# Kernel optimization log

Measured on AMD Instinct MI355X. Metric: run time of the kernel, lower is better.

The kernel has to match this reference:

```python
import jax, jax.numpy as jnp
import numpy as np

TAU = 0.2        # temperature
LAM = 0.5        # lambda_weight
P = 128          # proj_dim


def l2n(x):
    # tf.math.l2_normalize semantics: x / sqrt(max(sum(x^2), eps))
    return x / jnp.sqrt(jnp.maximum(jnp.sum(x * x, axis=-1, keepdims=True), 1e-12))


def global_head(feat, W1, b1, W2, b2):
    # GlobalAveragePooling2D -> Dense(2048, relu) -> Dense(128); dropout is identity in eval
    g = jnp.mean(feat, axis=(1, 2))                       # [B, C]
    return jax.nn.relu(g @ W1 + b1) @ W2 + b2             # [B, 128]


def dense_head(feat, W1, b1, W2, b2):
    # 1x1 Conv2D(2048, relu) -> 1x1 Conv2D(128) == per-pixel matmuls
    h = jax.nn.relu(jnp.einsum('bhwc,cd->bhwd', feat, W1) + b1)
    return jnp.einsum('bhwd,de->bhwe', h, W2) + b2        # [B, H, W, 128]


def dense_correspondence(q, k):
    b, h, w, c = q.shape
    f1 = q.reshape(b, h * w, c)
    f2 = k.reshape(b, h * w, c)
    sim = jnp.einsum('bnc,bmc->bnm', f1, f2)              # [B, hw, hw]
    idx = jnp.argmax(sim, axis=-1)                        # [B, hw]
    return jnp.take_along_axis(f2, idx[:, :, None], axis=1)  # batched gather


def info_nce(q, k):
    logits = (q @ k.T) / TAU                              # [N, N]
    lse = jax.nn.logsumexp(logits, axis=-1)
    pos = jnp.diagonal(logits)                            # labels = arange(N)
    return jnp.mean(lse - pos)


def queue_info_nce(q, k, queue):
    l_pos = jnp.sum(q * k, axis=-1, keepdims=True)        # [B, 1]
    l_neg = q @ queue.T                                   # [B, Q]
    logits = jnp.concatenate([l_pos, l_neg], axis=1) / TAU
    # labels are all zero -> positive logit is column 0
    return jnp.mean(jax.nn.logsumexp(logits, axis=-1) - logits[:, 0])


def setup_inputs() -> dict:
    key = jax.random.key(0)
    ks = jax.random.split(key, 16)
    B, H, W, C, D = 8, 28, 28, 1024, 2048
    Q = 65536
    s1 = 0.02
    inp = {
        'feat_q': jax.random.normal(ks[0], (B, H, W, C), jnp.float32),
        'feat_k': jax.random.normal(ks[1], (B, H, W, C), jnp.float32),
        'Wg1': jax.random.normal(ks[2], (C, D), jnp.float32) * s1,
        'bg1': jnp.zeros((D,), jnp.float32),
        'Wg2': jax.random.normal(ks[3], (D, P), jnp.float32) * s1,
        'bg2': jnp.zeros((P,), jnp.float32),
        'Wd1': jax.random.normal(ks[4], (C, D), jnp.float32) * s1,
        'bd1': jnp.zeros((D,), jnp.float32),
        'Wd2': jax.random.normal(ks[5], (D, P), jnp.float32) * s1,
        'bd2': jnp.zeros((P,), jnp.float32),
        'mWg1': jax.random.normal(ks[6], (C, D), jnp.float32) * s1,
        'mbg1': jnp.zeros((D,), jnp.float32),
        'mWg2': jax.random.normal(ks[7], (D, P), jnp.float32) * s1,
        'mbg2': jnp.zeros((P,), jnp.float32),
        'mWd1': jax.random.normal(ks[8], (C, D), jnp.float32) * s1,
        'mbd1': jnp.zeros((D,), jnp.float32),
        'mWd2': jax.random.normal(ks[9], (D, P), jnp.float32) * s1,
        'mbd2': jnp.zeros((P,), jnp.float32),
        'queue': l2n(jax.random.normal(ks[10], (Q, P), jnp.float32)),
    }
    return inp


def reference(feat_q, feat_k, Wg1, bg1, Wg2, bg2, Wd1, bd1, Wd2, bd2,
              mWg1, mbg1, mWg2, mbg2, mWd1, mbd1, mWd2, mbd2, queue):
    # student branch
    q_g = l2n(global_head(feat_q, Wg1, bg1, Wg2, bg2))
    q_d = l2n(dense_head(feat_q, Wd1, bd1, Wd2, bd2))
    # momentum (teacher) branch, stop-gradient as in train_step
    k_g = jax.lax.stop_gradient(l2n(global_head(feat_k, mWg1, mbg1, mWg2, mbg2)))
    k_d = jax.lax.stop_gradient(l2n(dense_head(feat_k, mWd1, mbd1, mWd2, mbd2)))
    # post-warmup path (warmup_epochs=0)
    l_g = queue_info_nce(q_g, k_g, queue)
    matched_k = dense_correspondence(q_d, k_d)
    l_d = info_nce(q_d.reshape(-1, P), matched_k.reshape(-1, P))
    total = (1.0 - LAM) * l_g + LAM * l_d
    return total
```

## Files before the change

### kernel.cpp

```cpp
#include <hip/hip_runtime.h>
#include <cstdint>

#define TAU_INV 5.0f
#define L2E 1.4426950408889634f

using ushort = unsigned short;
typedef __attribute__((ext_vector_type(8))) short s16x8;
typedef __attribute__((ext_vector_type(4))) float f32x4;

static __device__ __forceinline__ ushort f2bf(float x) {
  unsigned u = __float_as_uint(x);
  return (ushort)((u + 0x7fffu + ((u >> 16) & 1u)) >> 16);
}

static __device__ __forceinline__ float fexp2(float x) {
#if __has_builtin(__builtin_amdgcn_exp2f)
  return __builtin_amdgcn_exp2f(x);
#else
  return exp2f(x);
#endif
}

static __device__ __forceinline__ void gload_lds16(const void* g, void* l) {
  __builtin_amdgcn_global_load_lds(
      reinterpret_cast<const __attribute__((address_space(1))) void*>(
          reinterpret_cast<uintptr_t>(g)),
      reinterpret_cast<__attribute__((address_space(3))) void*>(
          (unsigned)reinterpret_cast<uintptr_t>(l)),
      16, 0, 0);
}

static __device__ __forceinline__ void xcd_swizzle(int gx, int gy, int& bx, int& by) {
  int nwg = gx * gy;
  int flat = by * gx + bx;
  int q = nwg >> 3, r = nwg & 7;
  int xcd = flat & 7, sl = flat >> 3;
  int tile = (xcd < r ? xcd * (q + 1) : r * (q + 1) + (xcd - r) * q) + sl;
  by = tile / gx;
  bx = tile - by * gx;
}

__global__ void k_cvt_pool(const float* __restrict__ fq, const float* __restrict__ fk,
                           ushort* __restrict__ obf, float* __restrict__ gpart) {
  int br = blockIdx.y >> 3, b = blockIdx.y & 7, pc = blockIdx.x, t = threadIdx.x;
  const float* feat = br ? fk : fq;
  const float* fp = feat + ((size_t)b * 784 + (size_t)pc * 7) * 1024;
  ushort* op = obf + (size_t)br * 6422528 + ((size_t)b * 784 + (size_t)pc * 7) * 1024;
  float4 acc = {0.f, 0.f, 0.f, 0.f};
#pragma unroll
  for (int p = 0; p < 7; ++p) {
    float4 v = ((const float4*)(fp + (size_t)p * 1024))[t];
    acc.x += v.x; acc.y += v.y; acc.z += v.z; acc.w += v.w;
    ushort4 r;
    r.x = f2bf(v.x); r.y = f2bf(v.y); r.z = f2bf(v.z); r.w = f2bf(v.w);
    ((ushort4*)(op + (size_t)p * 1024))[t] = r;
  }
  ((float4*)(gpart + ((size_t)blockIdx.y * 112 + pc) * 1024))[t] = acc;
}

__global__ void k_gpool_fin(const float* __restrict__ gpart, float* __restrict__ g) {
  int idx = blockIdx.x * 256 + threadIdx.x;
  int bb = idx >> 10, c = idx & 1023;
  float s = 0.f;
#pragma unroll 4
  for (int pc = 0; pc < 112; ++pc) s += gpart[((size_t)bb * 112 + pc) * 1024 + c];
  g[idx] = s * (1.0f / 784.0f);
}

__global__ void k_dense1_part(const float* __restrict__ g, const float* __restrict__ W0,
                              const float* __restrict__ W1, float* __restrict__ part1) {
  int br = blockIdx.z;
  const float* gb = g + (size_t)br * 8192;
  const float* W = br ? W1 : W0;
  float* p1 = part1 + (size_t)br * 262144;
  int d = blockIdx.x * 256 + threadIdx.x;
  int k0 = blockIdx.y * 64;
  __shared__ float gs[512];
  for (int i = threadIdx.x; i < 512; i += 256) gs[i] = gb[(i >> 6) * 1024 + k0 + (i & 63)];
  __syncthreads();
  float acc[8] = {};
  for (int kk = 0; kk < 64; ++kk) {
    float w = W[(size_t)(k0 + kk) * 2048 + d];
#pragma unroll
    for (int b = 0; b < 8; ++b) acc[b] += gs[b * 64 + kk] * w;
  }
#pragma unroll
  for (int b = 0; b < 8; ++b) p1[((size_t)blockIdx.y * 8 + b) * 2048 + d] = acc[b];
}

__global__ void k_d12(const float* __restrict__ part1, const float* __restrict__ b10,
                      const float* __restrict__ b11, const float* __restrict__ W20,
                      const float* __restrict__ W21, float* __restrict__ part2) {
  int br = blockIdx.y, k0 = blockIdx.x * 64;
  const float* p1 = part1 + (size_t)br * 262144;
  const float* b1 = br ? b11 : b10;
  const float* W2 = br ? W21 : W20;
  float* p2 = part2 + (size_t)br * 32768;
  __shared__ float hs[512];
  for (int i = threadIdx.x; i < 512; i += 128) {
    int b = i >> 6, kk = i & 63;
    float s = b1[k0 + kk];
#pragma unroll
    for (int ks = 0; ks < 16; ++ks) s += p1[((size_t)ks * 8 + b) * 2048 + k0 + kk];
    hs[i] = fmaxf(s, 0.f);
  }
  __syncthreads();
  int d = threadIdx.x;
  float acc[8] = {};
  for (int kk = 0; kk < 64; ++kk) {
    float w = W2[(size_t)(k0 + kk) * 128 + d];
#pragma unroll
    for (int b = 0; b < 8; ++b) acc[b] += hs[b * 64 + kk] * w;
  }
#pragma unroll
  for (int b = 0; b < 8; ++b) p2[((size_t)blockIdx.x * 8 + b) * 128 + d] = acc[b];
}

__global__ void k_head_fin(const float* __restrict__ p2q, const float* __restrict__ p2k,
                           const float* __restrict__ bq, const float* __restrict__ bk,
                           float* __restrict__ qg, float* __restrict__ kg,
                           float* __restrict__ lpos) {
  int b = blockIdx.x, lane = threadIdx.x;
  float q0 = bq[lane], q1 = bq[lane + 64];
  float k0 = bk[lane], k1 = bk[lane + 64];
#pragma unroll
  for (int s = 0; s < 32; ++s) {
    size_t base = ((size_t)s * 8 + b) * 128;
    q0 += p2q[base + lane]; q1 += p2q[base + lane + 64];
    k0 += p2k[base + lane]; k1 += p2k[base + lane + 64];
  }
  float sq = q0 * q0 + q1 * q1, sk = k0 * k0 + k1 * k1;
#pragma unroll
  for (int d = 1; d < 64; d <<= 1) { sq += __shfl_xor(sq, d); sk += __shfl_xor(sk, d); }
  float rq = 1.0f / sqrtf(fmaxf(sq, 1e-12f));
  float rk = 1.0f / sqrtf(fmaxf(sk, 1e-12f));
  q0 *= rq; q1 *= rq; k0 *= rk; k1 *= rk;
  qg[b * 128 + lane] = q0; qg[b * 128 + 64 + lane] = q1;
  kg[b * 128 + lane] = k0; kg[b * 128 + 64 + lane] = k1;
  float lp = q0 * k0 + q1 * k1;
#pragma unroll
  for (int d = 1; d < 64; d <<= 1) lp += __shfl_xor(lp, d);
  if (lane == 0) lpos[b] = lp;
}

__global__ void k_transpose_all(const float* __restrict__ Wd1, const float* __restrict__ mWd1,
                                const float* __restrict__ Wd2, const float* __restrict__ mWd2,
                                ushort* __restrict__ Wt1, ushort* __restrict__ Wt2) {
  int fl = blockIdx.x, z = blockIdx.z;
  const float* W;
  ushort* o;
  int bx, by, K, N;
  if (fl < 2048) {
    W = z ? mWd1 : Wd1;
    o = Wt1 + (size_t)z * 2097152;
    bx = fl & 63; by = fl >> 6; K = 1024; N = 2048;
  } else {
    fl -= 2048;
    W = z ? mWd2 : Wd2;
    o = Wt2 + (size_t)z * 262144;
    bx = fl & 3; by = fl >> 2; K = 2048; N = 128;
  }
  __shared__ float tile[32][33];
  int n0 = bx * 32, k0 = by * 32;
  int tx = threadIdx.x & 31, ty = threadIdx.x >> 5;
#pragma unroll
  for (int i = 0; i < 32; i += 8)
    tile[ty + i][tx] = W[(size_t)(k0 + ty + i) * N + n0 + tx];
  __syncthreads();
#pragma unroll
  for (int i = 0; i < 32; i += 8)
    o[(size_t)(n0 + ty + i) * K + k0 + tx] = f2bf(tile[tx][ty + i]);
}

__global__ __launch_bounds__(256) void k_gemm_e1(
    const ushort* __restrict__ A, long sA, const ushort* __restrict__ B, long sB,
    const float* __restrict__ bias0, const float* __restrict__ bias1,
    ushort* __restrict__ O, long sO, int K, int ldOut) {
  __shared__ unsigned char smem[65536];
  const int tid = threadIdx.x;
  int bx = blockIdx.x, by = blockIdx.y;
  const int bz = blockIdx.z;
  xcd_swizzle(gridDim.x, gridDim.y, bx, by);
  const ushort* Ab = A + (size_t)bz * sA;
  const ushort* Bb = B + (size_t)bz * sB;
  const float* bias = bz ? bias1 : bias0;
  ushort* Ob = O + (size_t)bz * sO;
  const int mBase = by * 128, nBase = bx * 128;
  const int lane = tid & 63;
  const int wid = tid >> 6;
  const int wid_u = __builtin_amdgcn_readfirstlane(wid);
  const int wm = wid >> 1, wn = wid & 1;
  const int lg = lane >> 4, li = lane & 15;
  const int lrow = lane >> 3, lchunk = lane & 7;

  const ushort* aSrc[4];
  const ushort* bSrc[4];
  int ldsOff[4];
#pragma unroll
  for (int j = 0; j < 4; ++j) {
    int r = wid_u * 32 + j * 8 + lrow;
    int gc = (lchunk ^ lrow) << 3;
    aSrc[j] = Ab + (size_t)(mBase + r) * K + gc;
    bSrc[j] = Bb + (size_t)(nBase + r) * K + gc;
    ldsOff[j] = (wid_u * 32 + j * 8) * 128;
  }
  f32x4 acc[4][4] = {};

  auto STAGE = [&](int buf, int k0) {
    unsigned base = (unsigned)buf * 32768u;
#pragma unroll
    for (int j = 0; j < 4; ++j) {
      gload_lds16(aSrc[j] + k0, smem + base + ldsOff[j]);
      gload_lds16(bSrc[j] + k0, smem + base + 16384 + ldsOff[j]);
    }
  };

  const int nt = K >> 6;
  STAGE(0, 0);
  __syncthreads();
  for (int t = 0; t < nt; ++t) {
    if (t + 1 < nt) STAGE((t + 1) & 1, (t + 1) << 6);
    const unsigned char* As = smem + (t & 1) * 32768;
    const unsigned char* Bs = As + 16384;
#pragma unroll
    for (int ks = 0; ks < 2; ++ks) {
      s16x8 af[4], bfr[4];
#pragma unroll
      for (int mi = 0; mi < 4; ++mi) {
        int r = wm * 64 + mi * 16 + li;
        af[mi] = *(const s16x8*)(const void*)(As + r * 128 + ((ks * 64 + lg * 16) ^ ((r & 7) << 4)));
      }
#pragma unroll
      for (int ni = 0; ni < 4; ++ni) {
        int c = wn * 64 + ni * 16 + li;
        bfr[ni] = *(const s16x8*)(const void*)(Bs + c * 128 + ((ks * 64 + lg * 16) ^ ((c & 7) << 4)));
      }
#pragma unroll
      for (int mi = 0; mi < 4; ++mi)
#pragma unroll
        for (int ni = 0; ni < 4; ++ni)
          acc[mi][ni] = __builtin_amdgcn_mfma_f32_16x16x32_bf16(af[mi], bfr[ni], acc[mi][ni], 0, 0, 0);
    }
    __syncthreads();
  }

#pragma unroll
  for (int ni = 0; ni < 4; ++ni) {
    int c = nBase + wn * 64 + ni * 16 + li;
    float bv = bias[c];
#pragma unroll
    for (int mi = 0; mi < 4; ++mi) {
#pragma unroll
      for (int rg = 0; rg < 4; ++rg) {
        int r = mBase + wm * 64 + mi * 16 + lg * 4 + rg;
        float v = fmaxf(acc[mi][ni][rg] + bv, 0.f);
        Ob[(size_t)r * ldOut + c] = f2bf(v);
      }
    }
  }
}

__global__ __launch_bounds__(256) void k_gemm_e2(
    const ushort* __restrict__ A, const ushort* __restrict__ B, float* __restrict__ o0,
    int Kloop, int lda, int ldb, long sA, long sB) {
  __shared__ unsigned char smem[65536];
  const int tid = threadIdx.x;
  int bx = blockIdx.x, by = blockIdx.y;
  const int bz = blockIdx.z;
  xcd_swizzle(gridDim.x, gridDim.y, bx, by);
  const ushort* Ab = A + (size_t)(bz >> 2) * sA + (size_t)(bz & 3) * Kloop;
  const ushort* Bb = B + (size_t)(bz >> 2) * sB + (size_t)(bz & 3) * Kloop;
  const int mBase = by * 128, nBase = bx * 128;
  const int lane = tid & 63;
  const int wid = tid >> 6;
  const int wid_u = __builtin_amdgcn_readfirstlane(wid);
  const int wm = wid >> 1, wn = wid & 1;
  const int lg = lane >> 4, li = lane & 15;
  const int lrow = lane >> 3, lchunk = lane & 7;

  const ushort* aSrc[4];
  const ushort* bSrc[4];
  int ldsOff[4];
#pragma unroll
  for (int j = 0; j < 4; ++j) {
    int r = wid_u * 32 + j * 8 + lrow;
    int gc = (lchunk ^ lrow) << 3;
    aSrc[j] = Ab + (size_t)(mBase + r) * lda + gc;
    bSrc[j] = Bb + (size_t)(nBase + r) * ldb + gc;
    ldsOff[j] = (wid_u * 32 + j * 8) * 128;
  }
  f32x4 acc[4][4] = {};

  auto STAGE = [&](int buf, int k0) {
    unsigned base = (unsigned)buf * 32768u;
#pragma unroll
    for (int j = 0; j < 4; ++j) {
      gload_lds16(aSrc[j] + k0, smem + base + ldsOff[j]);
      gload_lds16(bSrc[j] + k0, smem + base + 16384 + ldsOff[j]);
    }
  };

  const int nt = Kloop >> 6;
  STAGE(0, 0);
  __syncthreads();
  for (int t = 0; t < nt; ++t) {
    if (t + 1 < nt) STAGE((t + 1) & 1, (t + 1) << 6);
    const unsigned char* As = smem + (t & 1) * 32768;
    const unsigned char* Bs = As + 16384;
#pragma unroll
    for (int ks = 0; ks < 2; ++ks) {
      s16x8 af[4], bfr[4];
#pragma unroll
      for (int mi = 0; mi < 4; ++mi) {
        int r = wm * 64 + mi * 16 + li;
        af[mi] = *(const s16x8*)(const void*)(As + r * 128 + ((ks * 64 + lg * 16) ^ ((r & 7) << 4)));
      }
#pragma unroll
      for (int ni = 0; ni < 4; ++ni) {
        int c = wn * 64 + ni * 16 + li;
        bfr[ni] = *(const s16x8*)(const void*)(Bs + c * 128 + ((ks * 64 + lg * 16) ^ ((c & 7) << 4)));
      }
#pragma unroll
      for (int mi = 0; mi < 4; ++mi)
#pragma unroll
        for (int ni = 0; ni < 4; ++ni)
          acc[mi][ni] = __builtin_amdgcn_mfma_f32_16x16x32_bf16(af[mi], bfr[ni], acc[mi][ni], 0, 0, 0);
    }
    __syncthreads();
  }

#pragma unroll
  for (int ni = 0; ni < 4; ++ni) {
    int c = nBase + wn * 64 + ni * 16 + li;
#pragma unroll
    for (int mi = 0; mi < 4; ++mi)
#pragma unroll
      for (int rg = 0; rg < 4; ++rg) {
        int r = mBase + wm * 64 + mi * 16 + lg * 4 + rg;
        o0[(size_t)bz * 802816 + (size_t)r * 128 + c] = acc[mi][ni][rg];
      }
  }
}

template <int EPI>
__global__ __launch_bounds__(256) void k_gemm_k128(
    const ushort* __restrict__ A, const ushort* __restrict__ B,
    float* __restrict__ o0, int* __restrict__ o1,
    int Mvalid, int Nvalid, int ntiles, float scale, long sA, long sB) {
  __shared__ unsigned char smem[2048];
  const int tid = threadIdx.x;
  int bx = blockIdx.x, by = blockIdx.y;
  const int bz = blockIdx.z;
  xcd_swizzle(gridDim.x, gridDim.y, bx, by);
  const ushort* Ab = A + (size_t)bz * sA;
  const ushort* Bb = B + (size_t)bz * sB;
  const int mBase = by * 128, nBase = bx * 128;
  const int lane = tid & 63;
  const int wid = tid >> 6;
  const int wm = wid >> 1, wn = wid & 1;
  const int lg = lane >> 4, li = lane & 15;

  const ushort* aRow[4];
  const ushort* bCol[4];
#pragma unroll
  for (int mi = 0; mi < 4; ++mi) {
    int r = mBase + wm * 64 + mi * 16 + li;
    r = r < Mvalid ? r : Mvalid - 1;
    aRow[mi] = Ab + (size_t)r * 128 + lg * 8;
  }
#pragma unroll
  for (int ni = 0; ni < 4; ++ni) {
    int c = nBase + wn * 64 + ni * 16 + li;
    c = c < Nvalid ? c : Nvalid - 1;
    bCol[ni] = Bb + (size_t)c * 128 + lg * 8;
  }

  f32x4 acc[4][4] = {};
#pragma unroll
  for (int ks = 0; ks < 4; ++ks) {
    s16x8 af[4], bfr[4];
#pragma unroll
    for (int mi = 0; mi < 4; ++mi)
      af[mi] = *(const s16x8*)(const void*)(aRow[mi] + ks * 32);
#pragma unroll
    for (int ni = 0; ni < 4; ++ni)
      bfr[ni] = *(const s16x8*)(const void*)(bCol[ni] + ks * 32);
#pragma unroll
    for (int mi = 0; mi < 4; ++mi)
#pragma unroll
      for (int ni = 0; ni < 4; ++ni)
        acc[mi][ni] = __builtin_amdgcn_mfma_f32_16x16x32_bf16(af[mi], bfr[ni], acc[mi][ni], 0, 0, 0);
  }

  if constexpr (EPI == 2) {
    float* reds = (float*)(void*)smem;
#pragma unroll
    for (int mi = 0; mi < 4; ++mi)
#pragma unroll
      for (int rg = 0; rg < 4; ++rg) {
        float s = fexp2(acc[mi][0][rg] * scale) + fexp2(acc[mi][1][rg] * scale) +
                  fexp2(acc[mi][2][rg] * scale) + fexp2(acc[mi][3][rg] * scale);
#pragma unroll
        for (int d = 1; d < 16; d <<= 1) s += __shfl_xor(s, d);
        int rl = wm * 64 + mi * 16 + lg * 4 + rg;
        if (li == 0) reds[rl * 2 + wn] = s;
      }
    __syncthreads();
    if (tid < 128) {
      size_t idx = (size_t)(mBase + tid) * ntiles + bx;
      o0[idx] = reds[tid * 2] + reds[tid * 2 + 1];
    }
  } else {
    float* redv = (float*)(void*)smem;
    int* redi = (int*)(void*)(smem + 1024);
#pragma unroll
    for (int mi = 0; mi < 4; ++mi)
#pragma unroll
      for (int rg = 0; rg < 4; ++rg) {
        float bv = -3.4e38f;
        int bi = 0x7fffffff;
#pragma unroll
        for (int ni = 0; ni < 4; ++ni) {
          int c = nBase + wn * 64 + ni * 16 + li;
          float v = (c < Nvalid) ? acc[mi][ni][rg] : -3.4e38f;
          if (v > bv || (v == bv && c < bi)) { bv = v; bi = c; }
        }
#pragma unroll
        for (int d = 1; d < 16; d <<= 1) {
          float ov = __shfl_xor(bv, d);
          int oi = __shfl_xor(bi, d);
          if (ov > bv || (ov == bv && oi < bi)) { bv = ov; bi = oi; }
        }
        int rl = wm * 64 + mi * 16 + lg * 4 + rg;
        if (li == 0) { redv[rl * 2 + wn] = bv; redi[rl * 2 + wn] = bi; }
      }
    __syncthreads();
    if (tid < 128) {
      int r = mBase + tid;
      if (r < Mvalid) {
        float v0 = redv[tid * 2], v1 = redv[tid * 2 + 1];
        int i0 = redi[tid * 2], i1 = redi[tid * 2 + 1];
        float v = v0; int bi2 = i0;
        if (v1 > v || (v1 == v && i1 < bi2)) { v = v1; bi2 = i1; }
        size_t idx = (size_t)(bz * Mvalid + r) * ntiles + bx;
        o0[idx] = v;
        o1[idx] = bi2;
      }
    }
  }
}

__global__ void k_l2n_rows(const float* __restrict__ part, const float* __restrict__ bias0,
                           const float* __restrict__ bias1, float* __restrict__ of,
                           ushort* __restrict__ ob) {
  int br = blockIdx.y;
  const float* p = part + (size_t)br * 3211264;
  const float* bias = br ? bias1 : bias0;
  float* o = of + (size_t)br * 802816;
  ushort* o2 = ob + (size_t)br * 802816;
  int row = blockIdx.x * 4 + (threadIdx.x >> 6);
  int lane = threadIdx.x & 63;
  size_t i0 = (size_t)row * 128 + lane;
  const size_t SL = 802816;
  float v0 = bias[lane]      + p[i0]      + p[SL + i0]      + p[2 * SL + i0]      + p[3 * SL + i0];
  float v1 = bias[lane + 64] + p[i0 + 64] + p[SL + i0 + 64] + p[2 * SL + i0 + 64] + p[3 * SL + i0 + 64];
  float ss = v0 * v0 + v1 * v1;
#pragma unroll
  for (int d = 1; d < 64; d <<= 1) ss += __shfl_xor(ss, d);
  float r = 1.0f / sqrtf(fmaxf(ss, 1e-12f));
  o[i0] = v0 * r;
  o[i0 + 64] = v1 * r;
  o2[i0] = f2bf(v0 * r);
  o2[i0 + 64] = f2bf(v1 * r);
}

__global__ void k_argmax_gather(const float* __restrict__ pval, const int* __restrict__ pidx,
                                const ushort* __restrict__ kd_bf, ushort* __restrict__ matched_bf,
                                int* __restrict__ idxf) {
  int n = blockIdx.x;
  int b = n / 784;
  float bv = pval[(size_t)n * 7];
  int bi = pidx[(size_t)n * 7];
#pragma unroll
  for (int t = 1; t < 7; ++t) {
    float v = pval[(size_t)n * 7 + t];
    int i2 = pidx[(size_t)n * 7 + t];
    if (v > bv) { bv = v; bi = i2; }
  }
  int lane = threadIdx.x;
  if (lane == 0) idxf[n] = bi;
  const ushort* src = kd_bf + (size_t)(b * 784 + bi) * 128;
  ushort* dst = matched_bf + (size_t)n * 128;
  dst[lane] = src[lane];
  dst[lane + 64] = src[lane + 64];
}

__global__ __launch_bounds__(256) void k_qrow(const float* __restrict__ queue,
                                              const float* __restrict__ qg,
                                              float* __restrict__ ps,
                                              const float* __restrict__ psum,
                                              const int* __restrict__ idxf,
                                              const float* __restrict__ qd,
                                              const float* __restrict__ kd,
                                              float* __restrict__ diff) {
  __shared__ float qs[1024];
  __shared__ float lssum[8][4];
  int tid = threadIdx.x;
  int lane = tid & 63, w = tid >> 6;
  if (blockIdx.x < 256) {
    for (int i = tid; i < 1024; i += 256) qs[i] = qg[i];
    __syncthreads();
    int r = blockIdx.x * 256 + tid;
    const float* qr = queue + (size_t)r * 128;
    float a[8] = {0, 0, 0, 0, 0, 0, 0, 0};
    for (int j = 0; j < 128; j += 4) {
      float4 v = *(const float4*)(const void*)(qr + j);
#pragma unroll
      for (int b = 0; b < 8; ++b)
        a[b] += v.x * qs[b * 128 + j] + v.y * qs[b * 128 + j + 1] +
                v.z * qs[b * 128 + j + 2] + v.w * qs[b * 128 + j + 3];
    }
#pragma unroll
    for (int b = 0; b < 8; ++b) {
      float s = fexp2(a[b] * (TAU_INV * L2E));
#pragma unroll
      for (int d = 1; d < 64; d <<= 1) s += __shfl_xor(s, d);
      if (lane == 0) lssum[b][w] = s;
    }
    __syncthreads();
    if (tid < 8) {
      int b = tid;
      ps[blockIdx.x * 8 + b] = lssum[b][0] + lssum[b][1] + lssum[b][2] + lssum[b][3];
    }
  } else {
    int n = (blockIdx.x - 256) * 4 + w;
    float s = (lane < 49) ? psum[(size_t)n * 49 + lane] : 0.f;
#pragma unroll
    for (int d = 1; d < 64; d <<= 1) s += __shfl_xor(s, d);
    int b = n / 784;
    int mr = b * 784 + idxf[n];
    float pos = qd[(size_t)n * 128 + lane] * kd[(size_t)mr * 128 + lane] +
                qd[(size_t)n * 128 + 64 + lane] * kd[(size_t)mr * 128 + 64 + lane];
#pragma unroll
    for (int d = 1; d < 64; d <<= 1) pos += __shfl_xor(pos, d);
    if (lane == 0) diff[n] = logf(s) - pos * TAU_INV;
  }
}

__global__ void k_final(const float* __restrict__ ps, const float* __restrict__ lpos,
                        const float* __restrict__ diff, float* __restrict__ out) {
  int tid = threadIdx.x;
  int lane = tid & 63, w = tid >> 6;
  __shared__ float sm[4];
  float lg = 0.f;
  for (int b = 0; b < 8; ++b) {
    float s = ps[tid * 8 + b];
#pragma unroll
    for (int d = 1; d < 64; d <<= 1) s += __shfl_xor(s, d);
    if (lane == 0) sm[w] = s;
    __syncthreads();
    if (tid == 0) {
      float S = sm[0] + sm[1] + sm[2] + sm[3];
      float lp = lpos[b] * TAU_INV;
      S += fexp2(lp * L2E);
      lg += logf(S) - lp;
    }
    __syncthreads();
  }
  float v = 0.f;
  for (int i = tid; i < 6272; i += 256) v += diff[i];
#pragma unroll
  for (int d = 1; d < 64; d <<= 1) v += __shfl_xor(v, d);
  if (lane == 0) sm[w] = v;
  __syncthreads();
  if (tid == 0) {
    float ld = sm[0] + sm[1] + sm[2] + sm[3];
    out[0] = 0.5f * (lg * 0.125f) + 0.5f * (ld * (1.0f / 6272.0f));
  }
}

extern "C" void kernel_launch(void* const* d_in, const int* in_sizes, int n_in,
                              void* d_out, int out_size, void* d_ws, size_t ws_size,
                              hipStream_t stream) {
  (void)in_sizes; (void)n_in; (void)out_size; (void)ws_size;
  const float* feat_q = (const float*)d_in[0];
  const float* feat_k = (const float*)d_in[1];
  const float* Wg1 = (const float*)d_in[2];
  const float* bg1 = (const float*)d_in[3];
  const float* Wg2 = (const float*)d_in[4];
  const float* bg2 = (const float*)d_in[5];
  const float* Wd1 = (const float*)d_in[6];
  const float* bd1 = (const float*)d_in[7];
  const float* Wd2 = (const float*)d_in[8];
  const float* bd2 = (const float*)d_in[9];
  const float* mWg1 = (const float*)d_in[10];
  const float* mbg1 = (const float*)d_in[11];
  const float* mWg2 = (const float*)d_in[12];
  const float* mbg2 = (const float*)d_in[13];
  const float* mWd1 = (const float*)d_in[14];
  const float* mbd1 = (const float*)d_in[15];
  const float* mWd2 = (const float*)d_in[16];
  const float* mbd2 = (const float*)d_in[17];
  const float* queue = (const float*)d_in[18];
  float* out = (float*)d_out;

  char* ws = (char*)d_ws;
  size_t off = 0;
  auto alloc = [&](size_t bytes) -> void* {
    void* p = (void*)(ws + off);
    off += (bytes + 255) & ~(size_t)255;
    return p;
  };

  ushort* feat_bf = (ushort*)alloc(2ull * 6272 * 1024 * 2);
  ushort* Wd1t2 = (ushort*)alloc(2ull * 2048 * 1024 * 2);
  ushort* Wd2t2 = (ushort*)alloc(2ull * 128 * 2048 * 2);
  ushort* h_bf2 = (ushort*)alloc(2ull * 6272 * 2048 * 2);
  float* e2part2 = (float*)alloc(2ull * 4 * 6272 * 128 * 4);
  float* qdkd = (float*)alloc(2ull * 6272 * 128 * 4);
  ushort* qdkd_bf = (ushort*)alloc(2ull * 6272 * 128 * 2);
  ushort* matched_bf = (ushort*)alloc(6272ull * 128 * 2);
  float* psum = (float*)alloc(6272ull * 49 * 4);
  float* pval = (float*)alloc(6272ull * 7 * 4);
  int* pidx = (int*)alloc(6272ull * 7 * 4);
  int* idxf = (int*)alloc(6272ull * 4);
  float* gpart = (float*)alloc(16ull * 112 * 1024 * 4);
  float* g2 = (float*)alloc(2ull * 8 * 1024 * 4);
  float* part1 = (float*)alloc(2ull * 16 * 8 * 2048 * 4);
  float* part2 = (float*)alloc(2ull * 32 * 8 * 128 * 4);
  float* qg = (float*)alloc(8ull * 128 * 4);
  float* kg = (float*)alloc(8ull * 128 * 4);
  float* l_pos = (float*)alloc(8ull * 4);
  float* qpart_s = (float*)alloc(256ull * 8 * 4);
  float* diff = (float*)alloc(6272ull * 4);

  k_cvt_pool<<<dim3(112, 16), 256, 0, stream>>>(feat_q, feat_k, feat_bf, gpart);
  k_gpool_fin<<<64, 256, 0, stream>>>(gpart, g2);

  k_transpose_all<<<dim3(2304, 1, 2), 256, 0, stream>>>(Wd1, mWd1, Wd2, mWd2, Wd1t2, Wd2t2);

  k_dense1_part<<<dim3(8, 16, 2), 256, 0, stream>>>(g2, Wg1, mWg1, part1);
  k_d12<<<dim3(32, 2), 128, 0, stream>>>(part1, bg1, mbg1, Wg2, mWg2, part2);
  k_head_fin<<<8, 64, 0, stream>>>(part2, part2 + 32768, bg2, mbg2, qg, kg, l_pos);

  k_gemm_e1<<<dim3(16, 49, 2), 256, 0, stream>>>(feat_bf, 6422528, Wd1t2, 2097152,
                                                 bd1, mbd1, h_bf2, 12845056, 1024, 2048);
  k_gemm_e2<<<dim3(1, 49, 8), 256, 0, stream>>>(h_bf2, Wd2t2, e2part2,
                                                512, 2048, 2048, 12845056, 262144);
  k_l2n_rows<<<dim3(1568, 2), 256, 0, stream>>>(e2part2, bd2, mbd2, qdkd, qdkd_bf);

  k_gemm_k128<3><<<dim3(7, 7, 8), 256, 0, stream>>>(qdkd_bf, qdkd_bf + 802816, pval, pidx,
                                                    784, 784, 7, 0.f, 784l * 128, 784l * 128);
  k_argmax_gather<<<6272, 64, 0, stream>>>(pval, pidx, qdkd_bf + 802816, matched_bf, idxf);

  k_gemm_k128<2><<<dim3(49, 49, 1), 256, 0, stream>>>(qdkd_bf, matched_bf, psum, nullptr,
                                                      6272, 6272, 49, TAU_INV * L2E, 0, 0);

  k_qrow<<<1824, 256, 0, stream>>>(queue, qg, qpart_s, psum, idxf, qdkd, qdkd + 802816, diff);
  k_final<<<1, 256, 0, stream>>>(qpart_s, l_pos, diff, out);
}
```

Measured before the change: 228.7 us.

## Fuse small kernels and cut launches with last-block reductions and merged grids

Merges the feature conversion/pooling and weight transposes into one launch, folds the global-head first dense layer into the e1 GEMM grid as extra blocks, and finishes the global head (bias, normalise, positive logit) in the last block of the second dense kernel via an atomic counter. The e2 GEMM now does the split-K sum, bias and L2 normalisation in its last-arriving block per row tile. Correspondence argmax and gather become one kernel that loops over all column tiles, replacing the partial-argmax GEMM plus a separate gather. The goal is fewer launches and less intermediate traffic. The cost is atomic counters with a memset, serialized tail work in single blocks, and fewer blocks for the correspondence search.

```diff
diff --git a/kernel.cpp b/kernel.cpp
--- a/kernel.cpp
+++ b/kernel.cpp
@@ -40,22 +40,55 @@
   bx = tile - by * gx;
 }
 
-__global__ void k_cvt_pool(const float* __restrict__ fq, const float* __restrict__ fk,
-                           ushort* __restrict__ obf, float* __restrict__ gpart) {
-  int br = blockIdx.y >> 3, b = blockIdx.y & 7, pc = blockIdx.x, t = threadIdx.x;
-  const float* feat = br ? fk : fq;
-  const float* fp = feat + ((size_t)b * 784 + (size_t)pc * 7) * 1024;
-  ushort* op = obf + (size_t)br * 6422528 + ((size_t)b * 784 + (size_t)pc * 7) * 1024;
-  float4 acc = {0.f, 0.f, 0.f, 0.f};
-#pragma unroll
-  for (int p = 0; p < 7; ++p) {
-    float4 v = ((const float4*)(fp + (size_t)p * 1024))[t];
-    acc.x += v.x; acc.y += v.y; acc.z += v.z; acc.w += v.w;
-    ushort4 r;
-    r.x = f2bf(v.x); r.y = f2bf(v.y); r.z = f2bf(v.z); r.w = f2bf(v.w);
-    ((ushort4*)(op + (size_t)p * 1024))[t] = r;
-  }
-  ((float4*)(gpart + ((size_t)blockIdx.y * 112 + pc) * 1024))[t] = acc;
+__global__ void k_prep(const float* __restrict__ fq, const float* __restrict__ fk,
+                       ushort* __restrict__ obf, float* __restrict__ gpart,
+                       const float* __restrict__ Wd1, const float* __restrict__ mWd1,
+                       const float* __restrict__ Wd2, const float* __restrict__ mWd2,
+                       ushort* __restrict__ Wt1, ushort* __restrict__ Wt2) {
+  int bid = blockIdx.x;
+  if (bid < 1792) {
+    int pc = bid % 112, yy = bid / 112;
+    int br = yy >> 3, b = yy & 7, t = threadIdx.x;
+    const float* feat = br ? fk : fq;
+    const float* fp = feat + ((size_t)b * 784 + (size_t)pc * 7) * 1024;
+    ushort* op = obf + (size_t)br * 6422528 + ((size_t)b * 784 + (size_t)pc * 7) * 1024;
+    float4 acc = {0.f, 0.f, 0.f, 0.f};
+#pragma unroll
+    for (int p = 0; p < 7; ++p) {
+      float4 v = ((const float4*)(fp + (size_t)p * 1024))[t];
+      acc.x += v.x; acc.y += v.y; acc.z += v.z; acc.w += v.w;
+      ushort4 r;
+      r.x = f2bf(v.x); r.y = f2bf(v.y); r.z = f2bf(v.z); r.w = f2bf(v.w);
+      ((ushort4*)(op + (size_t)p * 1024))[t] = r;
+    }
+    ((float4*)(gpart + ((size_t)yy * 112 + pc) * 1024))[t] = acc;
+  } else {
+    int fl2 = bid - 1792;
+    int z = fl2 / 2304, fl = fl2 % 2304;
+    const float* W;
+    ushort* o;
+    int bx, by, K, N;
+    if (fl < 2048) {
+      W = z ? mWd1 : Wd1;
+      o = Wt1 + (size_t)z * 2097152;
+      bx = fl & 63; by = fl >> 6; K = 1024; N = 2048;
+    } else {
+      fl -= 2048;
+      W = z ? mWd2 : Wd2;
+      o = Wt2 + (size_t)z * 262144;
+      bx = fl & 3; by = fl >> 2; K = 2048; N = 128;
+    }
+    __shared__ float tile[32][33];
+    int n0 = bx * 32, k0 = by * 32;
+    int tx = threadIdx.x & 31, ty = threadIdx.x >> 5;
+#pragma unroll
+    for (int i = 0; i < 32; i += 8)
+      tile[ty + i][tx] = W[(size_t)(k0 + ty + i) * N + n0 + tx];
+    __syncthreads();
+#pragma unroll
+    for (int i = 0; i < 32; i += 8)
+      o[(size_t)(n0 + ty + i) * K + k0 + tx] = f2bf(tile[tx][ty + i]);
+  }
 }
 
 __global__ void k_gpool_fin(const float* __restrict__ gpart, float* __restrict__ g) {
@@ -67,119 +100,38 @@
   g[idx] = s * (1.0f / 784.0f);
 }
 
-__global__ void k_dense1_part(const float* __restrict__ g, const float* __restrict__ W0,
-                              const float* __restrict__ W1, float* __restrict__ part1) {
-  int br = blockIdx.z;
-  const float* gb = g + (size_t)br * 8192;
-  const float* W = br ? W1 : W0;
-  float* p1 = part1 + (size_t)br * 262144;
-  int d = blockIdx.x * 256 + threadIdx.x;
-  int k0 = blockIdx.y * 64;
-  __shared__ float gs[512];
-  for (int i = threadIdx.x; i < 512; i += 256) gs[i] = gb[(i >> 6) * 1024 + k0 + (i & 63)];
-  __syncthreads();
-  float acc[8] = {};
-  for (int kk = 0; kk < 64; ++kk) {
-    float w = W[(size_t)(k0 + kk) * 2048 + d];
-#pragma unroll
-    for (int b = 0; b < 8; ++b) acc[b] += gs[b * 64 + kk] * w;
-  }
-#pragma unroll
-  for (int b = 0; b < 8; ++b) p1[((size_t)blockIdx.y * 8 + b) * 2048 + d] = acc[b];
-}
-
-__global__ void k_d12(const float* __restrict__ part1, const float* __restrict__ b10,
-                      const float* __restrict__ b11, const float* __restrict__ W20,
-                      const float* __restrict__ W21, float* __restrict__ part2) {
-  int br = blockIdx.y, k0 = blockIdx.x * 64;
-  const float* p1 = part1 + (size_t)br * 262144;
-  const float* b1 = br ? b11 : b10;
-  const float* W2 = br ? W21 : W20;
-  float* p2 = part2 + (size_t)br * 32768;
-  __shared__ float hs[512];
-  for (int i = threadIdx.x; i < 512; i += 128) {
-    int b = i >> 6, kk = i & 63;
-    float s = b1[k0 + kk];
-#pragma unroll
-    for (int ks = 0; ks < 16; ++ks) s += p1[((size_t)ks * 8 + b) * 2048 + k0 + kk];
-    hs[i] = fmaxf(s, 0.f);
-  }
-  __syncthreads();
-  int d = threadIdx.x;
-  float acc[8] = {};
-  for (int kk = 0; kk < 64; ++kk) {
-    float w = W2[(size_t)(k0 + kk) * 128 + d];
-#pragma unroll
-    for (int b = 0; b < 8; ++b) acc[b] += hs[b * 64 + kk] * w;
-  }
-#pragma unroll
-  for (int b = 0; b < 8; ++b) p2[((size_t)blockIdx.x * 8 + b) * 128 + d] = acc[b];
-}
-
-__global__ void k_head_fin(const float* __restrict__ p2q, const float* __restrict__ p2k,
-                           const float* __restrict__ bq, const float* __restrict__ bk,
-                           float* __restrict__ qg, float* __restrict__ kg,
-                           float* __restrict__ lpos) {
-  int b = blockIdx.x, lane = threadIdx.x;
-  float q0 = bq[lane], q1 = bq[lane + 64];
-  float k0 = bk[lane], k1 = bk[lane + 64];
-#pragma unroll
-  for (int s = 0; s < 32; ++s) {
-    size_t base = ((size_t)s * 8 + b) * 128;
-    q0 += p2q[base + lane]; q1 += p2q[base + lane + 64];
-    k0 += p2k[base + lane]; k1 += p2k[base + lane + 64];
-  }
-  float sq = q0 * q0 + q1 * q1, sk = k0 * k0 + k1 * k1;
-#pragma unroll
-  for (int d = 1; d < 64; d <<= 1) { sq += __shfl_xor(sq, d); sk += __shfl_xor(sk, d); }
-  float rq = 1.0f / sqrtf(fmaxf(sq, 1e-12f));
-  float rk = 1.0f / sqrtf(fmaxf(sk, 1e-12f));
-  q0 *= rq; q1 *= rq; k0 *= rk; k1 *= rk;
-  qg[b * 128 + lane] = q0; qg[b * 128 + 64 + lane] = q1;
-  kg[b * 128 + lane] = k0; kg[b * 128 + 64 + lane] = k1;
-  float lp = q0 * k0 + q1 * k1;
-#pragma unroll
-  for (int d = 1; d < 64; d <<= 1) lp += __shfl_xor(lp, d);
-  if (lane == 0) lpos[b] = lp;
-}
-
-__global__ void k_transpose_all(const float* __restrict__ Wd1, const float* __restrict__ mWd1,
-                                const float* __restrict__ Wd2, const float* __restrict__ mWd2,
-                                ushort* __restrict__ Wt1, ushort* __restrict__ Wt2) {
-  int fl = blockIdx.x, z = blockIdx.z;
-  const float* W;
-  ushort* o;
-  int bx, by, K, N;
-  if (fl < 2048) {
-    W = z ? mWd1 : Wd1;
-    o = Wt1 + (size_t)z * 2097152;
-    bx = fl & 63; by = fl >> 6; K = 1024; N = 2048;
-  } else {
-    fl -= 2048;
-    W = z ? mWd2 : Wd2;
-    o = Wt2 + (size_t)z * 262144;
-    bx = fl & 3; by = fl >> 2; K = 2048; N = 128;
-  }
-  __shared__ float tile[32][33];
-  int n0 = bx * 32, k0 = by * 32;
-  int tx = threadIdx.x & 31, ty = threadIdx.x >> 5;
-#pragma unroll
-  for (int i = 0; i < 32; i += 8)
-    tile[ty + i][tx] = W[(size_t)(k0 + ty + i) * N + n0 + tx];
-  __syncthreads();
-#pragma unroll
-  for (int i = 0; i < 32; i += 8)
-    o[(size_t)(n0 + ty + i) * K + k0 + tx] = f2bf(tile[tx][ty + i]);
-}
-
-__global__ __launch_bounds__(256) void k_gemm_e1(
+__global__ __launch_bounds__(256) void k_e1d1(
     const ushort* __restrict__ A, long sA, const ushort* __restrict__ B, long sB,
     const float* __restrict__ bias0, const float* __restrict__ bias1,
-    ushort* __restrict__ O, long sO, int K, int ldOut) {
+    ushort* __restrict__ O, long sO, int K, int ldOut,
+    const float* __restrict__ g2, const float* __restrict__ Wg1,
+    const float* __restrict__ mWg1, float* __restrict__ part1) {
   __shared__ unsigned char smem[65536];
   const int tid = threadIdx.x;
+  const int bz = blockIdx.z;
+  if (bz == 2) {
+    int flat = blockIdx.y * 16 + blockIdx.x;
+    if (flat >= 256) return;
+    int dchunk = flat & 7, kslice = (flat >> 3) & 15, br = flat >> 7;
+    const float* gb = g2 + (size_t)br * 8192;
+    const float* W = br ? mWg1 : Wg1;
+    float* p1 = part1 + (size_t)br * 262144;
+    int d = dchunk * 256 + tid;
+    int k0 = kslice * 64;
+    float* gs = (float*)(void*)smem;
+    for (int i = tid; i < 512; i += 256) gs[i] = gb[(i >> 6) * 1024 + k0 + (i & 63)];
+    __syncthreads();
+    float acc[8] = {};
+    for (int kk = 0; kk < 64; ++kk) {
+      float w = W[(size_t)(k0 + kk) * 2048 + d];
+#pragma unroll
+      for (int b = 0; b < 8; ++b) acc[b] += gs[b * 64 + kk] * w;
+    }
+#pragma unroll
+    for (int b = 0; b < 8; ++b) p1[((size_t)kslice * 8 + b) * 2048 + d] = acc[b];
+    return;
+  }
   int bx = blockIdx.x, by = blockIdx.y;
-  const int bz = blockIdx.z;
   xcd_swizzle(gridDim.x, gridDim.y, bx, by);
   const ushort* Ab = A + (size_t)bz * sA;
   const ushort* Bb = B + (size_t)bz * sB;
@@ -260,16 +212,82 @@
   }
 }
 
-__global__ __launch_bounds__(256) void k_gemm_e2(
+__global__ void k_d12hf(const float* __restrict__ part1, const float* __restrict__ b10,
+                        const float* __restrict__ b11, const float* __restrict__ W20,
+                        const float* __restrict__ W21, float* __restrict__ part2,
+                        const float* __restrict__ bq, const float* __restrict__ bk,
+                        float* __restrict__ qg, float* __restrict__ kg,
+                        float* __restrict__ lpos, int* __restrict__ cnt) {
+  int br = blockIdx.y, k0 = blockIdx.x * 64;
+  const float* p1 = part1 + (size_t)br * 262144;
+  const float* b1 = br ? b11 : b10;
+  const float* W2 = br ? W21 : W20;
+  float* p2 = part2 + (size_t)br * 32768;
+  __shared__ float hs[512];
+  for (int i = threadIdx.x; i < 512; i += 128) {
+    int b = i >> 6, kk = i & 63;
+    float s = b1[k0 + kk];
+#pragma unroll
+    for (int ks = 0; ks < 16; ++ks) s += p1[((size_t)ks * 8 + b) * 2048 + k0 + kk];
+    hs[i] = fmaxf(s, 0.f);
+  }
+  __syncthreads();
+  int d = threadIdx.x;
+  float acc[8] = {};
+  for (int kk = 0; kk < 64; ++kk) {
+    float w = W2[(size_t)(k0 + kk) * 128 + d];
+#pragma unroll
+    for (int b = 0; b < 8; ++b) acc[b] += hs[b * 64 + kk] * w;
+  }
+#pragma unroll
+  for (int b = 0; b < 8; ++b) p2[((size_t)blockIdx.x * 8 + b) * 128 + d] = acc[b];
+
+  __threadfence();
+  __shared__ int lastf;
+  if (threadIdx.x == 0) lastf = (atomicAdd(cnt, 1) == 63) ? 1 : 0;
+  __syncthreads();
+  if (!lastf) return;
+  __threadfence();
+  const float* p2q = part2;
+  const float* p2k = part2 + 32768;
+  int lane = threadIdx.x & 63, w = threadIdx.x >> 6;
+  for (int b = w; b < 8; b += 2) {
+    float q0 = bq[lane], q1 = bq[lane + 64];
+    float k0v = bk[lane], k1 = bk[lane + 64];
+#pragma unroll
+    for (int s = 0; s < 32; ++s) {
+      size_t base = ((size_t)s * 8 + b) * 128;
+      q0 += p2q[base + lane]; q1 += p2q[base + lane + 64];
+      k0v += p2k[base + lane]; k1 += p2k[base + lane + 64];
+    }
+    float sq = q0 * q0 + q1 * q1, sk = k0v * k0v + k1 * k1;
+#pragma unroll
+    for (int dd = 1; dd < 64; dd <<= 1) { sq += __shfl_xor(sq, dd); sk += __shfl_xor(sk, dd); }
+    float rq = 1.0f / sqrtf(fmaxf(sq, 1e-12f));
+    float rk = 1.0f / sqrtf(fmaxf(sk, 1e-12f));
+    q0 *= rq; q1 *= rq; k0v *= rk; k1 *= rk;
+    qg[b * 128 + lane] = q0; qg[b * 128 + 64 + lane] = q1;
+    kg[b * 128 + lane] = k0v; kg[b * 128 + 64 + lane] = k1;
+    float lp = q0 * k0v + q1 * k1;
+#pragma unroll
+    for (int dd = 1; dd < 64; dd <<= 1) lp += __shfl_xor(lp, dd);
+    if (lane == 0) lpos[b] = lp;
+  }
+}
+
+__global__ __launch_bounds__(256) void k_e2l2n(
     const ushort* __restrict__ A, const ushort* __restrict__ B, float* __restrict__ o0,
-    int Kloop, int lda, int ldb, long sA, long sB) {
+    int Kloop, int lda, int ldb, long sA, long sB,
+    const float* __restrict__ bias0, const float* __restrict__ bias1,
+    float* __restrict__ of, ushort* __restrict__ ob, int* __restrict__ cnt) {
   __shared__ unsigned char smem[65536];
   const int tid = threadIdx.x;
   int bx = blockIdx.x, by = blockIdx.y;
   const int bz = blockIdx.z;
   xcd_swizzle(gridDim.x, gridDim.y, bx, by);
-  const ushort* Ab = A + (size_t)(bz >> 2) * sA + (size_t)(bz & 3) * Kloop;
-  const ushort* Bb = B + (size_t)(bz >> 2) * sB + (size_t)(bz & 3) * Kloop;
+  const int br = bz >> 2;
+  const ushort* Ab = A + (size_t)br * sA + (size_t)(bz & 3) * Kloop;
+  const ushort* Bb = B + (size_t)br * sB + (size_t)(bz & 3) * Kloop;
   const int mBase = by * 128, nBase = bx * 128;
   const int lane = tid & 63;
   const int wid = tid >> 6;
@@ -340,20 +358,149 @@
         o0[(size_t)bz * 802816 + (size_t)r * 128 + c] = acc[mi][ni][rg];
       }
   }
-}
-
-template <int EPI>
-__global__ __launch_bounds__(256) void k_gemm_k128(
-    const ushort* __restrict__ A, const ushort* __restrict__ B,
-    float* __restrict__ o0, int* __restrict__ o1,
-    int Mvalid, int Nvalid, int ntiles, float scale, long sA, long sB) {
-  __shared__ unsigned char smem[2048];
+
+  __threadfence();
+  __shared__ int lastf;
+  if (tid == 0) lastf = (atomicAdd(&cnt[br * 49 + by], 1) == 3) ? 1 : 0;
+  __syncthreads();
+  if (!lastf) return;
+  __threadfence();
+  const float* bias = br ? bias1 : bias0;
+  const float* p = o0 + (size_t)br * 3211264;
+  float* o = of + (size_t)br * 802816;
+  ushort* o2 = ob + (size_t)br * 802816;
+  int row = mBase + (tid >> 1);
+  int half = tid & 1;
+  size_t i0 = (size_t)row * 128 + half * 64;
+  const size_t SL = 802816;
+  float vs[64];
+  float ss = 0.f;
+#pragma unroll 16
+  for (int j = 0; j < 64; ++j) {
+    float v = bias[half * 64 + j] + p[i0 + j] + p[SL + i0 + j] + p[2 * SL + i0 + j] + p[3 * SL + i0 + j];
+    vs[j] = v;
+    ss += v * v;
+  }
+  ss += __shfl_xor(ss, 1);
+  float r = 1.0f / sqrtf(fmaxf(ss, 1e-12f));
+#pragma unroll 16
+  for (int j = 0; j < 64; ++j) {
+    float v = vs[j] * r;
+    o[i0 + j] = v;
+    o2[i0 + j] = f2bf(v);
+  }
+}
+
+__global__ __launch_bounds__(256) void k_corr(const ushort* __restrict__ qd_bf,
+                                              const ushort* __restrict__ kd_bf,
+                                              ushort* __restrict__ matched_bf,
+                                              int* __restrict__ idxf) {
+  __shared__ float redv[256];
+  __shared__ int redi[256];
+  __shared__ int finbi[128];
+  const int tid = threadIdx.x;
+  const int stripe = blockIdx.x, bat = blockIdx.y;
+  const ushort* Ab = qd_bf + (size_t)bat * 100352;
+  const ushort* Bb = kd_bf + (size_t)bat * 100352;
+  const int mBase = stripe * 128;
+  const int lane = tid & 63;
+  const int wid = tid >> 6;
+  const int wm = wid >> 1, wn = wid & 1;
+  const int lg = lane >> 4, li = lane & 15;
+
+  s16x8 af[4][4];
+#pragma unroll
+  for (int mi = 0; mi < 4; ++mi) {
+    int r = mBase + wm * 64 + mi * 16 + li;
+    r = r < 784 ? r : 783;
+#pragma unroll
+    for (int ks = 0; ks < 4; ++ks)
+      af[mi][ks] = *(const s16x8*)(const void*)(Ab + (size_t)r * 128 + ks * 32 + lg * 8);
+  }
+
+  float bv[4][4];
+  int bi[4][4];
+#pragma unroll
+  for (int mi = 0; mi < 4; ++mi)
+#pragma unroll
+    for (int rg = 0; rg < 4; ++rg) { bv[mi][rg] = -3.4e38f; bi[mi][rg] = 0x7fffffff; }
+
+  for (int ntile = 0; ntile < 7; ++ntile) {
+    int nBase = ntile * 128;
+    f32x4 acc[4][4] = {};
+#pragma unroll
+    for (int ks = 0; ks < 4; ++ks) {
+      s16x8 bfr[4];
+#pragma unroll
+      for (int ni = 0; ni < 4; ++ni) {
+        int c = nBase + wn * 64 + ni * 16 + li;
+        c = c < 784 ? c : 783;
+        bfr[ni] = *(const s16x8*)(const void*)(Bb + (size_t)c * 128 + ks * 32 + lg * 8);
+      }
+#pragma unroll
+      for (int mi = 0; mi < 4; ++mi)
+#pragma unroll
+        for (int ni = 0; ni < 4; ++ni)
+          acc[mi][ni] = __builtin_amdgcn_mfma_f32_16x16x32_bf16(af[mi][ks], bfr[ni], acc[mi][ni], 0, 0, 0);
+    }
+#pragma unroll
+    for (int mi = 0; mi < 4; ++mi)
+#pragma unroll
+      for (int rg = 0; rg < 4; ++rg) {
+        float tv = -3.4e38f;
+        int ti = 0x7fffffff;
+#pragma unroll
+        for (int ni = 0; ni < 4; ++ni) {
+          int c = nBase + wn * 64 + ni * 16 + li;
+          float v = (c < 784) ? acc[mi][ni][rg] : -3.4e38f;
+          if (v > tv || (v == tv && c < ti)) { tv = v; ti = c; }
+        }
+#pragma unroll
+        for (int d = 1; d < 16; d <<= 1) {
+          float ov = __shfl_xor(tv, d);
+          int oi = __shfl_xor(ti, d);
+          if (ov > tv || (ov == tv && oi < ti)) { tv = ov; ti = oi; }
+        }
+        if (tv > bv[mi][rg]) { bv[mi][rg] = tv; bi[mi][rg] = ti; }
+      }
+  }
+
+#pragma unroll
+  for (int mi = 0; mi < 4; ++mi)
+#pragma unroll
+    for (int rg = 0; rg < 4; ++rg) {
+      int rl = wm * 64 + mi * 16 + lg * 4 + rg;
+      if (li == 0) { redv[rl * 2 + wn] = bv[mi][rg]; redi[rl * 2 + wn] = bi[mi][rg]; }
+    }
+  __syncthreads();
+  if (tid < 128) {
+    int r = mBase + tid;
+    float v0 = redv[tid * 2], v1 = redv[tid * 2 + 1];
+    int i0 = redi[tid * 2], i1 = redi[tid * 2 + 1];
+    float v = v0; int b2 = i0;
+    if (v1 > v || (v1 == v && i1 < b2)) { v = v1; b2 = i1; }
+    finbi[tid] = b2;
+    if (r < 784) idxf[bat * 784 + r] = b2;
+  }
+  __syncthreads();
+  int rr = tid >> 1, half = tid & 1;
+  int r = mBase + rr;
+  if (r < 784) {
+    const ushort* src = Bb + (size_t)finbi[rr] * 128 + half * 64;
+    ushort* dst = matched_bf + ((size_t)bat * 784 + r) * 128 + half * 64;
+#pragma unroll
+    for (int j = 0; j < 4; ++j)
+      ((s16x8*)dst)[j] = ((const s16x8*)src)[j];
+  }
+}
+
+__global__ __launch_bounds__(256) void k_lse(const ushort* __restrict__ A,
+                                             const ushort* __restrict__ B,
+                                             float* __restrict__ o0, float scale) {
+  __shared__ float reds[256];
   const int tid = threadIdx.x;
   int bx = blockIdx.x, by = blockIdx.y;
-  const int bz = blockIdx.z;
   xcd_swizzle(gridDim.x, gridDim.y, bx, by);
-  const ushort* Ab = A + (size_t)bz * sA;
-  const ushort* Bb = B + (size_t)bz * sB;
   const int mBase = by * 128, nBase = bx * 128;
   const int lane = tid & 63;
   const int wid = tid >> 6;
@@ -363,17 +510,11 @@
   const ushort* aRow[4];
   const ushort* bCol[4];
 #pragma unroll
-  for (int mi = 0; mi < 4; ++mi) {
-    int r = mBase + wm * 64 + mi * 16 + li;
-    r = r < Mvalid ? r : Mvalid - 1;
-    aRow[mi] = Ab + (size_t)r * 128 + lg * 8;
-  }
-#pragma unroll
-  for (int ni = 0; ni < 4; ++ni) {
-    int c = nBase + wn * 64 + ni * 16 + li;
-    c = c < Nvalid ? c : Nvalid - 1;
-    bCol[ni] = Bb + (size_t)c * 128 + lg * 8;
-  }
+  for (int mi = 0; mi < 4; ++mi)
+    aRow[mi] = A + (size_t)(mBase + wm * 64 + mi * 16 + li) * 128 + lg * 8;
+#pragma unroll
+  for (int ni = 0; ni < 4; ++ni)
+    bCol[ni] = B + (size_t)(nBase + wn * 64 + ni * 16 + li) * 128 + lg * 8;
 
   f32x4 acc[4][4] = {};
 #pragma unroll
@@ -392,107 +533,22 @@
         acc[mi][ni] = __builtin_amdgcn_mfma_f32_16x16x32_bf16(af[mi], bfr[ni], acc[mi][ni], 0, 0, 0);
   }
 
-  if constexpr (EPI == 2) {
-    float* reds = (float*)(void*)smem;
-#pragma unroll
-    for (int mi = 0; mi < 4; ++mi)
-#pragma unroll
-      for (int rg = 0; rg < 4; ++rg) {
-        float s = fexp2(acc[mi][0][rg] * scale) + fexp2(acc[mi][1][rg] * scale) +
-                  fexp2(acc[mi][2][rg] * scale) + fexp2(acc[mi][3][rg] * scale);
-#pragma unroll
-        for (int d = 1; d < 16; d <<= 1) s += __shfl_xor(s, d);
-        int rl = wm * 64 + mi * 16 + lg * 4 + rg;
-        if (li == 0) reds[rl * 2 + wn] = s;
-      }
-    __syncthreads();
-    if (tid < 128) {
-      size_t idx = (size_t)(mBase + tid) * ntiles + bx;
-      o0[idx] = reds[tid * 2] + reds[tid * 2 + 1];
-    }
-  } else {
-    float* redv = (float*)(void*)smem;
-    int* redi = (int*)(void*)(smem + 1024);
-#pragma unroll
-    for (int mi = 0; mi < 4; ++mi)
-#pragma unroll
-      for (int rg = 0; rg < 4; ++rg) {
-        float bv = -3.4e38f;
-        int bi = 0x7fffffff;
-#pragma unroll
-        for (int ni = 0; ni < 4; ++ni) {
-          int c = nBase + wn * 64 + ni * 16 + li;
-          float v = (c < Nvalid) ? acc[mi][ni][rg] : -3.4e38f;
-          if (v > bv || (v == bv && c < bi)) { bv = v; bi = c; }
-        }
-#pragma unroll
-        for (int d = 1; d < 16; d <<= 1) {
-          float ov = __shfl_xor(bv, d);
-          int oi = __shfl_xor(bi, d);
-          if (ov > bv || (ov == bv && oi < bi)) { bv = ov; bi = oi; }
-        }
-        int rl = wm * 64 + mi * 16 + lg * 4 + rg;
-        if (li == 0) { redv[rl * 2 + wn] = bv; redi[rl * 2 + wn] = bi; }
-      }
-    __syncthreads();
-    if (tid < 128) {
-      int r = mBase + tid;
-      if (r < Mvalid) {
-        float v0 = redv[tid * 2], v1 = redv[tid * 2 + 1];
-        int i0 = redi[tid * 2], i1 = redi[tid * 2 + 1];
-        float v = v0; int bi2 = i0;
-        if (v1 > v || (v1 == v && i1 < bi2)) { v = v1; bi2 = i1; }
-        size_t idx = (size_t)(bz * Mvalid + r) * ntiles + bx;
-        o0[idx] = v;
-        o1[idx] = bi2;
-      }
-    }
-  }
-}
-
-__global__ void k_l2n_rows(const float* __restrict__ part, const float* __restrict__ bias0,
-                           const float* __restrict__ bias1, float* __restrict__ of,
-                           ushort* __restrict__ ob) {
-  int br = blockIdx.y;
-  const float* p = part + (size_t)br * 3211264;
-  const float* bias = br ? bias1 : bias0;
-  float* o = of + (size_t)br * 802816;
-  ushort* o2 = ob + (size_t)br * 802816;
-  int row = blockIdx.x * 4 + (threadIdx.x >> 6);
-  int lane = threadIdx.x & 63;
-  size_t i0 = (size_t)row * 128 + lane;
-  const size_t SL = 802816;
-  float v0 = bias[lane]      + p[i0]      + p[SL + i0]      + p[2 * SL + i0]      + p[3 * SL + i0];
-  float v1 = bias[lane + 64] + p[i0 + 64] + p[SL + i0 + 64] + p[2 * SL + i0 + 64] + p[3 * SL + i0 + 64];
-  float ss = v0 * v0 + v1 * v1;
-#pragma unroll
-  for (int d = 1; d < 64; d <<= 1) ss += __shfl_xor(ss, d);
-  float r = 1.0f / sqrtf(fmaxf(ss, 1e-12f));
-  o[i0] = v0 * r;
-  o[i0 + 64] = v1 * r;
-  o2[i0] = f2bf(v0 * r);
-  o2[i0 + 64] = f2bf(v1 * r);
-}
-
-__global__ void k_argmax_gather(const float* __restrict__ pval, const int* __restrict__ pidx,
-                                const ushort* __restrict__ kd_bf, ushort* __restrict__ matched_bf,
-                                int* __restrict__ idxf) {
-  int n = blockIdx.x;
-  int b = n / 784;
-  float bv = pval[(size_t)n * 7];
-  int bi = pidx[(size_t)n * 7];
-#pragma unroll
-  for (int t = 1; t < 7; ++t) {
-    float v = pval[(size_t)n * 7 + t];
-    int i2 = pidx[(size_t)n * 7 + t];
-    if (v > bv) { bv = v; bi = i2; }
-  }
-  int lane = threadIdx.x;
-  if (lane == 0) idxf[n] = bi;
-  const ushort* src = kd_bf + (size_t)(b * 784 + bi) * 128;
-  ushort* dst = matched_bf + (size_t)n * 128;
-  dst[lane] = src[lane];
-  dst[lane + 64] = src[lane + 64];
+#pragma unroll
+  for (int mi = 0; mi < 4; ++mi)
+#pragma unroll
+    for (int rg = 0; rg < 4; ++rg) {
+      float s = fexp2(acc[mi][0][rg] * scale) + fexp2(acc[mi][1][rg] * scale) +
+                fexp2(acc[mi][2][rg] * scale) + fexp2(acc[mi][3][rg] * scale);
+#pragma unroll
+      for (int d = 1; d < 16; d <<= 1) s += __shfl_xor(s, d);
+      int rl = wm * 64 + mi * 16 + lg * 4 + rg;
+      if (li == 0) reds[rl * 2 + wn] = s;
+    }
+  __syncthreads();
+  if (tid < 128) {
+    size_t idx = (size_t)(mBase + tid) * 49 + bx;
+    o0[idx] = reds[tid * 2] + reds[tid * 2 + 1];
+  }
 }
 
 __global__ __launch_bounds__(256) void k_qrow(const float* __restrict__ queue,
@@ -621,8 +677,6 @@
   ushort* qdkd_bf = (ushort*)alloc(2ull * 6272 * 128 * 2);
   ushort* matched_bf = (ushort*)alloc(6272ull * 128 * 2);
   float* psum = (float*)alloc(6272ull * 49 * 4);
-  float* pval = (float*)alloc(6272ull * 7 * 4);
-  int* pidx = (int*)alloc(6272ull * 7 * 4);
   int* idxf = (int*)alloc(6272ull * 4);
   float* gpart = (float*)alloc(16ull * 112 * 1024 * 4);
   float* g2 = (float*)alloc(2ull * 8 * 1024 * 4);
@@ -633,28 +687,27 @@
   float* l_pos = (float*)alloc(8ull * 4);
   float* qpart_s = (float*)alloc(256ull * 8 * 4);
   float* diff = (float*)alloc(6272ull * 4);
-
-  k_cvt_pool<<<dim3(112, 16), 256, 0, stream>>>(feat_q, feat_k, feat_bf, gpart);
+  int* cnt = (int*)alloc(512);
+
+  hipMemsetAsync(cnt, 0, 512, stream);
+
+  k_prep<<<6400, 256, 0, stream>>>(feat_q, feat_k, feat_bf, gpart,
+                                   Wd1, mWd1, Wd2, mWd2, Wd1t2, Wd2t2);
   k_gpool_fin<<<64, 256, 0, stream>>>(gpart, g2);
 
-  k_transpose_all<<<dim3(2304, 1, 2), 256, 0, stream>>>(Wd1, mWd1, Wd2, mWd2, Wd1t2, Wd2t2);
-
-  k_dense1_part<<<dim3(8, 16, 2), 256, 0, stream>>>(g2, Wg1, mWg1, part1);
-  k_d12<<<dim3(32, 2), 128, 0, stream>>>(part1, bg1, mbg1, Wg2, mWg2, part2);
-  k_head_fin<<<8, 64, 0, stream>>>(part2, part2 + 32768, bg2, mbg2, qg, kg, l_pos);
-
-  k_gemm_e1<<<dim3(16, 49, 2), 256, 0, stream>>>(feat_bf, 6422528, Wd1t2, 2097152,
-                                                 bd1, mbd1, h_bf2, 12845056, 1024, 2048);
-  k_gemm_e2<<<dim3(1, 49, 8), 256, 0, stream>>>(h_bf2, Wd2t2, e2part2,
-                                                512, 2048, 2048, 12845056, 262144);
-  k_l2n_rows<<<dim3(1568, 2), 256, 0, stream>>>(e2part2, bd2, mbd2, qdkd, qdkd_bf);
-
-  k_gemm_k128<3><<<dim3(7, 7, 8), 256, 0, stream>>>(qdkd_bf, qdkd_bf + 802816, pval, pidx,
-                                                    784, 784, 7, 0.f, 784l * 128, 784l * 128);
-  k_argmax_gather<<<6272, 64, 0, stream>>>(pval, pidx, qdkd_bf + 802816, matched_bf, idxf);
-
-  k_gemm_k128<2><<<dim3(49, 49, 1), 256, 0, stream>>>(qdkd_bf, matched_bf, psum, nullptr,
-                                                      6272, 6272, 49, TAU_INV * L2E, 0, 0);
+  k_e1d1<<<dim3(16, 49, 3), 256, 0, stream>>>(feat_bf, 6422528, Wd1t2, 2097152,
+                                              bd1, mbd1, h_bf2, 12845056, 1024, 2048,
+                                              g2, Wg1, mWg1, part1);
+  k_d12hf<<<dim3(32, 2), 128, 0, stream>>>(part1, bg1, mbg1, Wg2, mWg2, part2,
+                                           bg2, mbg2, qg, kg, l_pos, cnt);
+
+  k_e2l2n<<<dim3(1, 49, 8), 256, 0, stream>>>(h_bf2, Wd2t2, e2part2,
+                                              512, 2048, 2048, 12845056, 262144,
+                                              bd2, mbd2, qdkd, qdkd_bf, cnt + 1);
+
+  k_corr<<<dim3(7, 8), 256, 0, stream>>>(qdkd_bf, qdkd_bf + 802816, matched_bf, idxf);
+
+  k_lse<<<dim3(49, 49), 256, 0, stream>>>(qdkd_bf, matched_bf, psum, TAU_INV * L2E);
 
   k_qrow<<<1824, 256, 0, stream>>>(queue, qg, qpart_s, psum, idxf, qdkd, qdkd + 802816, diff);
   k_final<<<1, 256, 0, stream>>>(qpart_s, l_pos, diff, out);
```

Result: slower. 457.7 us (+100.2%).
